# Optimization experiments

Measured on AMD Instinct MI355X. Metric: run time of the kernel, lower is better.

Reference implementation:

```python
import jax, jax.numpy as jnp
import numpy as np

N_ATOMS = 50000
N_BONDS = 100000
MAX_NB = 6
ATOM_FDIM = 133
BOND_FDIM = 147
HIDDEN = 512
DEPTH = 5
N_MOLS = 2048


def setup_inputs() -> dict:
    key = jax.random.key(0)
    ks = jax.random.split(key, 10)
    f_atoms = jax.random.normal(ks[0], (N_ATOMS, ATOM_FDIM), dtype=jnp.float32)
    f_bonds = jax.random.normal(ks[1], (N_BONDS, BOND_FDIM), dtype=jnp.float32)
    a2b = jax.random.randint(ks[2], (N_ATOMS, MAX_NB), 0, N_BONDS, dtype=jnp.int32)
    b2a = jax.random.randint(ks[3], (N_BONDS,), 0, N_ATOMS, dtype=jnp.int32)
    # reverse bond of directed bond i is its pair i^1 (chemprop layout)
    b2revb = (jnp.arange(N_BONDS, dtype=jnp.int32) ^ 1)
    mol_ids = jnp.sort(jax.random.randint(ks[4], (N_ATOMS,), 0, N_MOLS, dtype=jnp.int32))
    W_i = jax.random.normal(ks[5], (BOND_FDIM, HIDDEN), dtype=jnp.float32) * 0.05
    W_h = jax.random.normal(ks[6], (HIDDEN, HIDDEN), dtype=jnp.float32) * 0.05
    W_o = jax.random.normal(ks[7], (ATOM_FDIM + HIDDEN, HIDDEN), dtype=jnp.float32) * 0.05
    b_o = jnp.zeros((HIDDEN,), dtype=jnp.float32)
    return {"f_atoms": f_atoms, "f_bonds": f_bonds, "a2b": a2b, "b2a": b2a,
            "b2revb": b2revb, "mol_ids": mol_ids, "W_i": W_i, "W_h": W_h,
            "W_o": W_o, "b_o": b_o, "n_mols": N_MOLS}


def _dmpnn_forward(f_atoms, f_bonds, a2b, b2a, b2revb, mol_ids,
                   W_i, W_h, W_o, b_o, n_mols):
    # input = W_i(f_bonds); message = act(input)   (bond messages, bias=False)
    inp = f_bonds @ W_i                      # [n_bonds, H]
    message = jax.nn.relu(inp)
    for _ in range(DEPTH - 1):
        nei = message[a2b]                   # gather: [n_atoms, max_nb, H]
        a_message = nei.sum(axis=1)          # [n_atoms, H]
        rev_message = message[b2revb]        # [n_bonds, H]
        message = a_message[b2a] - rev_message
        message = jax.nn.relu(inp + message @ W_h)
    # final atom aggregation
    nei = message[a2b]                       # [n_atoms, max_nb, H]
    a_message = nei.sum(axis=1)              # [n_atoms, H]
    a_input = jnp.concatenate([f_atoms, a_message], axis=1)
    atom_hiddens = jax.nn.relu(a_input @ W_o + b_o)   # [n_atoms, H]
    # scope-based mean aggregation per molecule (== a_scope loop, mean)
    sums = jax.ops.segment_sum(atom_hiddens, mol_ids, num_segments=n_mols)
    counts = jax.ops.segment_sum(jnp.ones((atom_hiddens.shape[0],), atom_hiddens.dtype),
                                 mol_ids, num_segments=n_mols)
    mol_vecs = jnp.where(counts[:, None] > 0, sums / jnp.maximum(counts, 1.0)[:, None], 0.0)
    return mol_vecs


def reference(f_atoms, f_bonds, a2b, b2a, b2revb, mol_ids, W_i, W_h, W_o, b_o, n_mols):
    return _dmpnn_forward(f_atoms, f_bonds, a2b, b2a, b2revb, mol_ids,
                          W_i, W_h, W_o, b_o, n_mols)
```

## Files before the change

kernel.cpp:

```cpp
#include <hip/hip_runtime.h>

typedef unsigned int u32;
typedef unsigned short u16;

constexpr int N_ATOMS   = 50000;
constexpr int N_BONDS   = 100000;
constexpr int MAX_NB    = 6;
constexpr int ATOM_FDIM = 133;
constexpr int BOND_FDIM = 147;
constexpr int HIDDEN    = 512;
constexpr int DEPTH     = 5;
constexpr int N_MOLS    = 2048;
constexpr int KB_PAD    = 160;
constexpr int KC        = 672;

typedef short bf16x8 __attribute__((ext_vector_type(8)));
typedef float f32x4  __attribute__((ext_vector_type(4)));

__device__ __forceinline__ float b2f(u32 u) {
    u <<= 16; float f; __builtin_memcpy(&f, &u, 4); return f;
}
__device__ __forceinline__ u16 f2b(float f) {
    u32 u; __builtin_memcpy(&u, &f, 4);
    u = (u + 0x7fffu + ((u >> 16) & 1u)) >> 16;
    return (u16)u;
}
__device__ __forceinline__ u32 pack2(float x, float y) {
    return (u32)f2b(x) | ((u32)f2b(y) << 16);
}
__device__ __forceinline__ float load_in(const void* p, size_t i, u32 bf) {
    return bf ? b2f((u32)((const u16*)p)[i]) : ((const float*)p)[i];
}

__global__ void k_detect(const void* fb, u32* flag) {
    if (threadIdx.x == 0 && blockIdx.x == 0) {
        const u16* p = (const u16*)fb;
        int cnt = 0;
        for (int i = 0; i < 64; ++i) {
            const u32 e = (p[i] >> 7) & 0xFF;
            if (e >= 110 && e <= 140) ++cnt;
        }
        *flag = (cnt >= 52) ? 1u : 0u;
    }
}

template <int SPLIT, int MODE>
__global__ void gemm_bt(const u16* __restrict__ A, int ldaA,
                        const u16* __restrict__ A2,
                        const u16* __restrict__ BT, int ldb,
                        const u16* __restrict__ bias,
                        u16* __restrict__ out,
                        int M, int K)
{
    __shared__ u16 As[128 * 32];
    __shared__ u16 Bs[128 * 32];
    const int g    = blockIdx.x;
    const int mt   = (g >> 5) * 8 + (g & 7);
    const int nt   = (g >> 3) & 3;
    const int bm0  = mt * 128;
    if (bm0 >= M) return;
    const int bn0  = nt * 128;
    const int t    = threadIdx.x;
    const int w    = t >> 6;
    const int l    = t & 63;
    const int quad = l >> 4;
    const int lr   = l & 15;
    const int wr   = (w >> 1) * 64;
    const int wc   = (w & 1) * 64;

    f32x4 acc[4][4];
#pragma unroll
    for (int i = 0; i < 4; ++i)
#pragma unroll
        for (int j = 0; j < 4; ++j) acc[i][j] = (f32x4){0.f, 0.f, 0.f, 0.f};

    const int kt_n = K >> 5;
    for (int kt = 0; kt < kt_n; ++kt) {
        const int k0 = kt << 5;
        const u16* srcA;
        int lda, kcol;
        if (SPLIT && kt >= 5) { srcA = A2; lda = HIDDEN; kcol = k0 - KB_PAD; }
        else                  { srcA = A;  lda = ldaA;   kcol = k0; }
        __syncthreads();
#pragma unroll
        for (int j = 0; j < 2; ++j) {
            const int cj = w + j * 4;
            const int c  = cj * 64 + l;
            const int r  = c >> 2;
            const int kg = (c & 3) ^ ((r >> 1) & 3);
            int rowA = bm0 + r; if (rowA >= M) rowA = M - 1;
            const u16* ga = srcA + (size_t)rowA * lda + kcol + kg * 8;
            __builtin_amdgcn_global_load_lds(
                (const __attribute__((address_space(1))) void*)ga,
                (__attribute__((address_space(3))) void*)(As + cj * 512),
                16, 0, 0);
            const int rowB = bn0 + r;
            const u16* gb = BT + (size_t)rowB * ldb + k0 + kg * 8;
            __builtin_amdgcn_global_load_lds(
                (const __attribute__((address_space(1))) void*)gb,
                (__attribute__((address_space(3))) void*)(Bs + cj * 512),
                16, 0, 0);
        }
        __syncthreads();

        bf16x8 af[4], bfr[4];
#pragma unroll
        for (int i = 0; i < 4; ++i) {
            const int ra = wr + i * 16 + lr;
            const int rb = wc + i * 16 + lr;
            af[i]  = *(const bf16x8*)(As + ra * 32 + (quad ^ ((ra >> 1) & 3)) * 8);
            bfr[i] = *(const bf16x8*)(Bs + rb * 32 + (quad ^ ((rb >> 1) & 3)) * 8);
        }
#pragma unroll
        for (int i = 0; i < 4; ++i)
#pragma unroll
            for (int j = 0; j < 4; ++j)
                acc[i][j] = __builtin_amdgcn_mfma_f32_16x16x32_bf16(
                    af[i], bfr[j], acc[i][j], 0, 0, 0);
    }

#pragma unroll
    for (int i = 0; i < 4; ++i) {
        const int row0 = bm0 + wr + i * 16 + quad * 4;
#pragma unroll
        for (int j = 0; j < 4; ++j) {
            const int col = bn0 + wc + j * 16 + lr;
#pragma unroll
            for (int r = 0; r < 4; ++r) {
                const int row = row0 + r;
                if (row < M) {
                    float v = acc[i][j][r];
                    if (MODE == 1) v += b2f((u32)bias[col]);
                    out[(size_t)row * HIDDEN + col] = f2b(v > 0.f ? v : 0.f);
                }
            }
        }
    }
}

static inline int gemm_grid(int M) { return (((M + 127) / 128 + 7) & ~7) * 4; }

__global__ void k_pad_bonds(const void* __restrict__ src,
                            u16* __restrict__ dst,
                            const u32* __restrict__ flag)
{
    const u32 bf = *flag;
    const int idx = blockIdx.x * 256 + threadIdx.x;
    if (idx >= N_BONDS * KB_PAD) return;
    const int b = idx / KB_PAD, k = idx - b * KB_PAD;
    dst[idx] = (k < BOND_FDIM) ? f2b(load_in(src, (size_t)b * BOND_FDIM + k, bf))
                               : (u16)0;
}

__global__ void k_wcT(const void* __restrict__ wi,
                      const void* __restrict__ wh,
                      u16* __restrict__ wt,
                      const u32* __restrict__ flag)
{
    const u32 bf = *flag;
    const int idx = blockIdx.x * 256 + threadIdx.x;
    if (idx >= 512 * KC) return;
    const int n = idx / KC, k = idx - n * KC;
    float v = 0.f;
    if (k < BOND_FDIM)    v = load_in(wi, (size_t)k * HIDDEN + n, bf);
    else if (k >= KB_PAD) v = load_in(wh, (size_t)(k - KB_PAD) * HIDDEN + n, bf);
    wt[idx] = f2b(v);
}

__global__ void k_woT(const void* __restrict__ wo,
                      u16* __restrict__ wt,
                      const u32* __restrict__ flag)
{
    const u32 bf = *flag;
    const int idx = blockIdx.x * 256 + threadIdx.x;
    if (idx >= 512 * KC) return;
    const int n = idx / KC, k = idx - n * KC;
    float v = 0.f;
    if (k < HIDDEN)                  v = load_in(wo, (size_t)(ATOM_FDIM + k) * HIDDEN + n, bf);
    else if (k < HIDDEN + ATOM_FDIM) v = load_in(wo, (size_t)(k - HIDDEN) * HIDDEN + n, bf);
    wt[idx] = f2b(v);
}

__global__ void k_bias(const void* __restrict__ b, u16* __restrict__ dst,
                       const u32* __restrict__ flag)
{
    const u32 bf = *flag;
    const int i = threadIdx.x + blockIdx.x * 256;
    if (i < HIDDEN) dst[i] = f2b(load_in(b, i, bf));
}

__device__ __forceinline__ void acc_row(float* acc, const uint4 v, float s) {
    acc[0] += s * b2f(v.x & 0xffffu); acc[1] += s * b2f(v.x >> 16);
    acc[2] += s * b2f(v.y & 0xffffu); acc[3] += s * b2f(v.y >> 16);
    acc[4] += s * b2f(v.z & 0xffffu); acc[5] += s * b2f(v.z >> 16);
    acc[6] += s * b2f(v.w & 0xffffu); acc[7] += s * b2f(v.w >> 16);
}

__global__ void k_pre(const u16* __restrict__ message,
                      const int* __restrict__ a2b,
                      const int* __restrict__ b2a,
                      const int* __restrict__ b2revb,
                      u16* __restrict__ pre)
{
    const int b = blockIdx.x * 4 + (threadIdx.x >> 6);
    const int l = threadIdx.x & 63;
    const int a  = b2a[b];
    const int rb = b2revb[b];
    float acc[8] = {0.f, 0.f, 0.f, 0.f, 0.f, 0.f, 0.f, 0.f};
    acc_row(acc, *(const uint4*)(message + (size_t)rb * HIDDEN + l * 8), -1.f);
#pragma unroll
    for (int j = 0; j < MAX_NB; ++j) {
        const int nb = a2b[a * MAX_NB + j];
        acc_row(acc, *(const uint4*)(message + (size_t)nb * HIDDEN + l * 8), 1.f);
    }
    uint4 o;
    o.x = pack2(acc[0], acc[1]); o.y = pack2(acc[2], acc[3]);
    o.z = pack2(acc[4], acc[5]); o.w = pack2(acc[6], acc[7]);
    *(uint4*)(pre + (size_t)b * HIDDEN + l * 8) = o;
}

__global__ void k_amsg(const u16* __restrict__ message,
                       const int* __restrict__ a2b,
                       u16* __restrict__ ain)
{
    const int a = blockIdx.x * 4 + (threadIdx.x >> 6);
    const int l = threadIdx.x & 63;
    float acc[8] = {0.f, 0.f, 0.f, 0.f, 0.f, 0.f, 0.f, 0.f};
#pragma unroll
    for (int j = 0; j < MAX_NB; ++j) {
        const int nb = a2b[a * MAX_NB + j];
        acc_row(acc, *(const uint4*)(message + (size_t)nb * HIDDEN + l * 8), 1.f);
    }
    uint4 o;
    o.x = pack2(acc[0], acc[1]); o.y = pack2(acc[2], acc[3]);
    o.z = pack2(acc[4], acc[5]); o.w = pack2(acc[6], acc[7]);
    *(uint4*)(ain + (size_t)a * KC + l * 8) = o;
}

__global__ void k_atomfill(const void* __restrict__ f_atoms,
                           u16* __restrict__ ain,
                           const u32* __restrict__ flag)
{
    const u32 bf = *flag;
    const int idx = blockIdx.x * 256 + threadIdx.x;
    if (idx >= N_ATOMS * (KC - HIDDEN)) return;
    const int a = idx / (KC - HIDDEN), c = idx - a * (KC - HIDDEN);
    u16 v = 0;
    if (c < ATOM_FDIM) v = f2b(load_in(f_atoms, (size_t)a * ATOM_FDIM + c, bf));
    ain[(size_t)a * KC + HIDDEN + c] = v;
}

__global__ void k_mean(const u16* __restrict__ ah,
                       const int* __restrict__ mol_ids,
                       void* __restrict__ out,
                       const u32* __restrict__ flag)
{
    const u32 bf = *flag;
    const int m = blockIdx.x, t = threadIdx.x;
    int lo = 0, hi = N_ATOMS;
    while (lo < hi) { const int mid = (lo + hi) >> 1; if (mol_ids[mid] < m) lo = mid + 1; else hi = mid; }
    const int start = lo;
    hi = N_ATOMS;
    while (lo < hi) { const int mid = (lo + hi) >> 1; if (mol_ids[mid] <= m) lo = mid + 1; else hi = mid; }
    const int end = lo;
    float x = 0.f, y = 0.f;
    for (int a = start; a < end; ++a) {
        const u32 p = *(const u32*)(ah + (size_t)a * HIDDEN + t * 2);
        x += b2f(p & 0xffffu); y += b2f(p >> 16);
    }
    const float inv = (end > start) ? 1.f / (float)(end - start) : 0.f;
    x *= inv; y *= inv;
    if (bf) {
        *(u32*)((u16*)out + (size_t)m * HIDDEN + t * 2) = pack2(x, y);
    } else {
        float* o = (float*)out + (size_t)m * HIDDEN + t * 2;
        o[0] = x; o[1] = y;
    }
}

extern "C" void kernel_launch(void* const* d_in, const int* in_sizes, int n_in,
                              void* d_out, int out_size, void* d_ws, size_t ws_size,
                              hipStream_t stream)
{
    const void* f_atoms = d_in[0];
    const void* f_bonds = d_in[1];
    const int* a2b     = (const int*)d_in[2];
    const int* b2a     = (const int*)d_in[3];
    const int* b2revb  = (const int*)d_in[4];
    const int* mol_ids = (const int*)d_in[5];
    const void* W_i = d_in[6];
    const void* W_h = d_in[7];
    const void* W_o = d_in[8];
    const void* b_o = d_in[9];

    char* ws = (char*)d_ws;
    size_t off = 0;
    auto alloc = [&](size_t bytes) -> char* {
        char* p = ws + off;
        off += (bytes + 255) & ~(size_t)255;
        return p;
    };
    u32* flag     = (u32*)alloc(256);
    u16* biasB    = (u16*)alloc((size_t)HIDDEN * 2);
    u16* WcT      = (u16*)alloc((size_t)512 * KC * 2);
    u16* WoT      = (u16*)alloc((size_t)512 * KC * 2);
    u16* fbpad    = (u16*)alloc((size_t)N_BONDS * KB_PAD * 2);
    u16* pre      = (u16*)alloc((size_t)N_BONDS * HIDDEN * 2);
    u16* message  = (u16*)alloc((size_t)N_BONDS * HIDDEN * 2);
    u16* ain = pre;
    u16* ah  = message;

    k_detect<<<dim3(1), 64, 0, stream>>>(f_bonds, flag);
    k_wcT<<<dim3((512 * KC + 255) / 256), 256, 0, stream>>>(W_i, W_h, WcT, flag);
    k_woT<<<dim3((512 * KC + 255) / 256), 256, 0, stream>>>(W_o, WoT, flag);
    k_bias<<<dim3(2), 256, 0, stream>>>(b_o, biasB, flag);
    k_pad_bonds<<<dim3((N_BONDS * KB_PAD + 255) / 256), 256, 0, stream>>>(f_bonds, fbpad, flag);

    const dim3 gB(gemm_grid(N_BONDS));
    gemm_bt<1, 0><<<gB, 256, 0, stream>>>(fbpad, KB_PAD, pre, WcT, KC, nullptr,
                                          message, N_BONDS, KB_PAD);
    for (int d = 0; d < DEPTH - 1; ++d) {
        k_pre<<<dim3(N_BONDS / 4), 256, 0, stream>>>(message, a2b, b2a, b2revb, pre);
        gemm_bt<1, 0><<<gB, 256, 0, stream>>>(fbpad, KB_PAD, pre, WcT, KC, nullptr,
                                              message, N_BONDS, KC);
    }
    k_amsg<<<dim3(N_ATOMS / 4), 256, 0, stream>>>(message, a2b, ain);
    k_atomfill<<<dim3((N_ATOMS * (KC - HIDDEN) + 255) / 256), 256, 0, stream>>>(f_atoms, ain, flag);
    gemm_bt<0, 1><<<dim3(gemm_grid(N_ATOMS)), 256, 0, stream>>>(
        ain, KC, nullptr, WoT, KC, biasB, ah, N_ATOMS, KC);
    k_mean<<<dim3(N_MOLS), 256, 0, stream>>>(ah, mol_ids, d_out, flag);
}
```

Before: 1.155 ms.

## Group bonds by source atom via CSR to reuse neighbor sums in k_pre

Builds a CSR from b2a (count, scan, scatter) once per call. The per-bond pre-message kernel becomes per-atom: each atom sums its six neighbor messages once, then writes (sum - reverse message) for every bond whose source is that atom. This is meant to remove the redundant six-row gather done per bond, cutting gather traffic about in half. In exchange it adds setup kernels with atomics and an uneven per-atom loop, and the bond write order now depends on the atomic scatter order.

```diff
diff --git a/kernel.cpp b/kernel.cpp
--- a/kernel.cpp
+++ b/kernel.cpp
@@ -189,6 +189,50 @@
     if (i < HIDDEN) dst[i] = f2b(load_in(b, i, bf));
 }
 
+__global__ void k_zero(u32* p, int n) {
+    const int i = blockIdx.x * 256 + threadIdx.x;
+    if (i < n) p[i] = 0;
+}
+__global__ void k_count(const int* __restrict__ b2a, u32* __restrict__ cnt) {
+    const int b = blockIdx.x * 256 + threadIdx.x;
+    if (b < N_BONDS) atomicAdd(&cnt[b2a[b]], 1u);
+}
+__global__ void k_scan(const u32* __restrict__ cnt, u32* __restrict__ off) {
+    __shared__ u32 part[1024];
+    __shared__ u32 carry;
+    const int t = threadIdx.x;
+    constexpr int CH = (N_ATOMS + 1023) / 1024;
+    u32 local[CH];
+    u32 s = 0;
+    for (int j = 0; j < CH; ++j) {
+        const int i = t * CH + j;
+        local[j] = s;
+        if (i < N_ATOMS) s += cnt[i];
+    }
+    part[t] = s;
+    __syncthreads();
+    if (t == 0) {
+        u32 run = 0;
+        for (int i = 0; i < 1024; ++i) { const u32 v = part[i]; part[i] = run; run += v; }
+        carry = run;
+    }
+    __syncthreads();
+    const u32 base = part[t];
+    for (int j = 0; j < CH; ++j) {
+        const int i = t * CH + j;
+        if (i < N_ATOMS) off[i] = base + local[j];
+    }
+    if (t == 0) off[N_ATOMS] = carry;
+}
+__global__ void k_scatter(const int* __restrict__ b2a,
+                          u32* __restrict__ pos, u32* __restrict__ csr) {
+    const int b = blockIdx.x * 256 + threadIdx.x;
+    if (b < N_BONDS) {
+        const u32 p = atomicAdd(&pos[b2a[b]], 1u);
+        csr[p] = (u32)b;
+    }
+}
+
 __device__ __forceinline__ void acc_row(float* acc, const uint4 v, float s) {
     acc[0] += s * b2f(v.x & 0xffffu); acc[1] += s * b2f(v.x >> 16);
     acc[2] += s * b2f(v.y & 0xffffu); acc[3] += s * b2f(v.y >> 16);
@@ -196,27 +240,35 @@
     acc[6] += s * b2f(v.w & 0xffffu); acc[7] += s * b2f(v.w >> 16);
 }
 
-__global__ void k_pre(const u16* __restrict__ message,
-                      const int* __restrict__ a2b,
-                      const int* __restrict__ b2a,
-                      const int* __restrict__ b2revb,
-                      u16* __restrict__ pre)
-{
-    const int b = blockIdx.x * 4 + (threadIdx.x >> 6);
+__global__ void k_pre_g(const u16* __restrict__ message,
+                        const int* __restrict__ a2b,
+                        const u32* __restrict__ csr,
+                        const u32* __restrict__ off,
+                        const int* __restrict__ b2revb,
+                        u16* __restrict__ pre)
+{
+    const int a = blockIdx.x * 4 + (threadIdx.x >> 6);
+    if (a >= N_ATOMS) return;
     const int l = threadIdx.x & 63;
-    const int a  = b2a[b];
-    const int rb = b2revb[b];
+    const int s = (int)off[a], e = (int)off[a + 1];
+    if (s == e) return;
     float acc[8] = {0.f, 0.f, 0.f, 0.f, 0.f, 0.f, 0.f, 0.f};
-    acc_row(acc, *(const uint4*)(message + (size_t)rb * HIDDEN + l * 8), -1.f);
 #pragma unroll
     for (int j = 0; j < MAX_NB; ++j) {
         const int nb = a2b[a * MAX_NB + j];
         acc_row(acc, *(const uint4*)(message + (size_t)nb * HIDDEN + l * 8), 1.f);
     }
-    uint4 o;
-    o.x = pack2(acc[0], acc[1]); o.y = pack2(acc[2], acc[3]);
-    o.z = pack2(acc[4], acc[5]); o.w = pack2(acc[6], acc[7]);
-    *(uint4*)(pre + (size_t)b * HIDDEN + l * 8) = o;
+    for (int i = s; i < e; ++i) {
+        const int b  = (int)csr[i];
+        const int rb = b2revb[b];
+        const uint4 vm = *(const uint4*)(message + (size_t)rb * HIDDEN + l * 8);
+        uint4 o;
+        o.x = pack2(acc[0] - b2f(vm.x & 0xffffu), acc[1] - b2f(vm.x >> 16));
+        o.y = pack2(acc[2] - b2f(vm.y & 0xffffu), acc[3] - b2f(vm.y >> 16));
+        o.z = pack2(acc[4] - b2f(vm.z & 0xffffu), acc[5] - b2f(vm.z >> 16));
+        o.w = pack2(acc[6] - b2f(vm.w & 0xffffu), acc[7] - b2f(vm.w >> 16));
+        *(uint4*)(pre + (size_t)b * HIDDEN + l * 8) = o;
+    }
 }
 
 __global__ void k_amsg(const u16* __restrict__ message,
@@ -294,16 +346,20 @@
     const void* b_o = d_in[9];
 
     char* ws = (char*)d_ws;
-    size_t off = 0;
+    size_t off_ = 0;
     auto alloc = [&](size_t bytes) -> char* {
-        char* p = ws + off;
-        off += (bytes + 255) & ~(size_t)255;
+        char* p = ws + off_;
+        off_ += (bytes + 255) & ~(size_t)255;
         return p;
     };
     u32* flag     = (u32*)alloc(256);
     u16* biasB    = (u16*)alloc((size_t)HIDDEN * 2);
     u16* WcT      = (u16*)alloc((size_t)512 * KC * 2);
     u16* WoT      = (u16*)alloc((size_t)512 * KC * 2);
+    u32* cnt      = (u32*)alloc((size_t)N_ATOMS * 4);
+    u32* offs     = (u32*)alloc((size_t)(N_ATOMS + 1) * 4);
+    u32* pos      = (u32*)alloc((size_t)N_ATOMS * 4);
+    u32* csr      = (u32*)alloc((size_t)N_BONDS * 4);
     u16* fbpad    = (u16*)alloc((size_t)N_BONDS * KB_PAD * 2);
     u16* pre      = (u16*)alloc((size_t)N_BONDS * HIDDEN * 2);
     u16* message  = (u16*)alloc((size_t)N_BONDS * HIDDEN * 2);
@@ -316,11 +372,19 @@
     k_bias<<<dim3(2), 256, 0, stream>>>(b_o, biasB, flag);
     k_pad_bonds<<<dim3((N_BONDS * KB_PAD + 255) / 256), 256, 0, stream>>>(f_bonds, fbpad, flag);
 
+    k_zero<<<dim3((N_ATOMS + 255) / 256), 256, 0, stream>>>(cnt, N_ATOMS);
+    k_count<<<dim3((N_BONDS + 255) / 256), 256, 0, stream>>>(b2a, cnt);
+    k_scan<<<dim3(1), 1024, 0, stream>>>(cnt, offs);
+    k_zero<<<dim3((N_ATOMS + 255) / 256), 256, 0, stream>>>(pos, N_ATOMS);
+    hipMemcpyAsync(pos, offs, (size_t)N_ATOMS * 4, hipMemcpyDeviceToDevice, stream);
+    k_scatter<<<dim3((N_BONDS + 255) / 256), 256, 0, stream>>>(b2a, pos, csr);
+
     const dim3 gB(gemm_grid(N_BONDS));
     gemm_bt<1, 0><<<gB, 256, 0, stream>>>(fbpad, KB_PAD, pre, WcT, KC, nullptr,
                                           message, N_BONDS, KB_PAD);
     for (int d = 0; d < DEPTH - 1; ++d) {
-        k_pre<<<dim3(N_BONDS / 4), 256, 0, stream>>>(message, a2b, b2a, b2revb, pre);
+        k_pre_g<<<dim3((N_ATOMS + 3) / 4), 256, 0, stream>>>(
+            message, a2b, csr, offs, b2revb, pre);
         gemm_bt<1, 0><<<gB, 256, 0, stream>>>(fbpad, KB_PAD, pre, WcT, KC, nullptr,
                                               message, N_BONDS, KC);
     }
```

Result: faster. 1.054 ms (-8.7%).
